# Kernel tuning notes

Measured on AMD Instinct MI355X. Metric: run time of the kernel, lower is better.

## Reference

```python
import jax, jax.numpy as jnp
import numpy as np

H = 64          # HIDDEN_DIM
V = 64          # VOCAB_SIZE
SLOTS = 8       # MEMORY_SLOTS
B, L = 256, 2048
LN_EPS = 1e-5
THRESH = 1.5    # entropy_threshold


def setup_inputs() -> dict:
    key = jax.random.key(0)
    ks = jax.random.split(key, 14)
    s = 0.05
    return {
        "seq": jax.random.randint(ks[0], (B, L), 0, V),
        "embed": jax.random.normal(ks[1], (V, H), jnp.float32) * s,
        "w1": jax.random.normal(ks[2], (H, 2 * H), jnp.float32) * s,
        "b1": jax.random.normal(ks[3], (2 * H,), jnp.float32) * s,
        "w2": jax.random.normal(ks[4], (2 * H, H), jnp.float32) * s,
        "b2": jax.random.normal(ks[5], (H,), jnp.float32) * s,
        "ln_g": jnp.ones((H,), jnp.float32),
        "ln_b": jnp.zeros((H,), jnp.float32),
        "gate_w": jax.random.normal(ks[6], (H, 1), jnp.float32) * s,
        "gate_b": jax.random.normal(ks[7], (1,), jnp.float32) * s,
        "q_w": jax.random.normal(ks[8], (H, H), jnp.float32) * s,
        "q_b": jax.random.normal(ks[9], (H,), jnp.float32) * s,
        "out_w": jax.random.normal(ks[10], (H, V), jnp.float32) * s,
        "out_b": jax.random.normal(ks[11], (V,), jnp.float32) * s,
    }


def reference(seq, embed, w1, b1, w2, b2, ln_g, ln_b,
              gate_w, gate_b, q_w, q_b, out_w, out_b):
    # Encoder: embed + FFN residual + LayerNorm
    h0 = embed[seq]                                      # [B, L, H]
    ff = jnp.maximum(h0 @ w1 + b1, 0.0) @ w2 + b2        # [B, L, H]
    z = h0 + ff
    mu = z.mean(-1, keepdims=True)
    var = z.var(-1, keepdims=True)
    h = (z - mu) / jnp.sqrt(var + LN_EPS) * ln_g + ln_b  # [B, L, H]

    # Top-k gate scores -> gather memory slots
    scores = (h @ gate_w)[..., 0] + gate_b[0]            # [B, L]
    _, idx = jax.lax.top_k(scores, SLOTS)                # [B, SLOTS]
    memory = jnp.take_along_axis(h, idx[:, :, None], axis=1)  # [B, SLOTS, H]

    # Tiny attention from last-token query over memory slots
    q = h[:, -1, :] @ q_w + q_b                          # [B, H]
    logits_attn = jnp.einsum('bkh,bh->bk', memory, q) / (H ** 0.5)
    attn = jax.nn.softmax(logits_attn, axis=-1)          # [B, SLOTS]

    # Entropy gate: fall back to uniform attention when entropy is high
    entropy = -(attn * jnp.log(attn + 1e-9)).sum(-1)     # [B]
    high = (entropy > THRESH).astype(attn.dtype)[:, None]
    eff_attn = (1.0 - high) * attn + high * (1.0 / SLOTS)

    ctx = jnp.einsum('bk,bkh->bh', eff_attn, memory)     # [B, H]
    logits = ctx @ out_w + out_b                         # [B, V]
    return logits, entropy.mean()
```

## Files before the change

### kernel.cpp

```cpp
#include <hip/hip_runtime.h>

#define HID 64
#define VOC 64
#define NSLOT 8
#define NB 256
#define SEQL 2048

__global__ __launch_bounds__(64) void vocab_kernel(
    const float* __restrict__ embed, const float* __restrict__ w1, const float* __restrict__ b1,
    const float* __restrict__ w2, const float* __restrict__ b2,
    const float* __restrict__ ln_g, const float* __restrict__ ln_b,
    const float* __restrict__ gate_w, const float* __restrict__ gate_b,
    const float* __restrict__ q_w, const float* __restrict__ q_b,
    float* __restrict__ wsH, float* __restrict__ wsQ, float* __restrict__ wsScore,
    float* __restrict__ ent_out)
{
    const int lane = threadIdx.x;
    const int v = blockIdx.x;

    if (v == 0 && lane == 0) ent_out[0] = 0.0f;

    const float e = embed[v * HID + lane];

    float fa = b1[lane], fb = b1[HID + lane];
#pragma unroll
    for (int i = 0; i < HID; ++i) {
        const float ei = __shfl(e, i);
        fa = fmaf(ei, w1[i * 2 * HID + lane], fa);
        fb = fmaf(ei, w1[i * 2 * HID + HID + lane], fb);
    }
    fa = fmaxf(fa, 0.0f);
    fb = fmaxf(fb, 0.0f);

    float za = e + b2[lane], zb = 0.0f;
#pragma unroll
    for (int j = 0; j < HID; ++j) {
        za = fmaf(__shfl(fa, j), w2[j * HID + lane], za);
        zb = fmaf(__shfl(fb, j), w2[(HID + j) * HID + lane], zb);
    }
    const float z = za + zb;

    float s = z;
#pragma unroll
    for (int m = 32; m; m >>= 1) s += __shfl_xor(s, m);
    const float mu = s * (1.0f / HID);
    const float d = z - mu;
    float vs = d * d;
#pragma unroll
    for (int m = 32; m; m >>= 1) vs += __shfl_xor(vs, m);
    const float inv = 1.0f / sqrtf(vs * (1.0f / HID) + 1e-5f);
    const float h = d * inv * ln_g[lane] + ln_b[lane];
    wsH[v * HID + lane] = h;

    float sc = h * gate_w[lane];
#pragma unroll
    for (int m = 32; m; m >>= 1) sc += __shfl_xor(sc, m);
    if (lane == 0) wsScore[v] = sc + gate_b[0];

    float q = q_b[lane];
#pragma unroll
    for (int k = 0; k < HID; ++k)
        q = fmaf(__shfl(h, k), q_w[k * HID + lane], q);
    wsQ[v * HID + lane] = q;
}

__global__ __launch_bounds__(256) void batch_kernel(
    const int* __restrict__ seq,
    const float* __restrict__ out_w, const float* __restrict__ out_b,
    const float* __restrict__ wsH, const float* __restrict__ wsQ,
    const float* __restrict__ wsScore,
    float* __restrict__ out, float* __restrict__ ent_out)
{
    __shared__ int hist[VOC];
    __shared__ float sscore[VOC];
    __shared__ float hlds[VOC * (HID + 1)];
    __shared__ float sqv[HID];
    __shared__ int sorder[VOC];
    __shared__ int svids[NSLOT];
    __shared__ float sla[NSLOT];
    __shared__ float seff[NSLOT];
    __shared__ int shvlast;

    const int t = threadIdx.x;
    const int b = blockIdx.x;

    if (t < VOC) { hist[t] = 0; sscore[t] = wsScore[t]; }
    if (t == 0) shvlast = seq[(size_t)b * SEQL + SEQL - 1];
    __syncthreads();

    const int4* row4 = (const int4*)(seq + (size_t)b * SEQL);
    for (int p = t; p < SEQL / 4; p += 256) {
        const int4 vv = row4[p];
        atomicAdd(&hist[vv.x], 1);
        atomicAdd(&hist[vv.y], 1);
        atomicAdd(&hist[vv.z], 1);
        atomicAdd(&hist[vv.w], 1);
    }
    for (int p = t; p < VOC * HID; p += 256)
        hlds[(p >> 6) * (HID + 1) + (p & 63)] = wsH[p];
    __syncthreads();

    if (t < VOC) {
        const float sv = sscore[t];
        int r = 0;
        for (int u = 0; u < VOC; ++u) {
            const float su = sscore[u];
            if (su > sv || (su == sv && u < t)) ++r;
        }
        sorder[r] = t;
        sqv[t] = wsQ[shvlast * HID + t];
    }
    __syncthreads();

    if (t == 0) {
        int r = NSLOT, n = 0, pos = 0;
        while (r > 0) {
            const int v = sorder[pos++];
            int c = hist[v];
            if (c > r) c = r;
            for (int k = 0; k < c; ++k) svids[n++] = v;
            r -= c;
        }
    }
    __syncthreads();

    if (t < NSLOT) {
        const float* hr = &hlds[svids[t] * (HID + 1)];
        float acc = 0.0f;
#pragma unroll
        for (int i = 0; i < HID; ++i) acc = fmaf(hr[i], sqv[i], acc);
        sla[t] = acc * 0.125f;
    }
    __syncthreads();

    if (t == 0) {
        float m = -1e30f;
        for (int k = 0; k < NSLOT; ++k) m = fmaxf(m, sla[k]);
        float e[NSLOT], s = 0.0f;
        for (int k = 0; k < NSLOT; ++k) { e[k] = expf(sla[k] - m); s += e[k]; }
        const float invs = 1.0f / s;
        float ent = 0.0f;
        for (int k = 0; k < NSLOT; ++k) {
            const float a = e[k] * invs;
            ent -= a * logf(a + 1e-9f);
        }
        const float high = (ent > 1.5f) ? 1.0f : 0.0f;
        for (int k = 0; k < NSLOT; ++k)
            seff[k] = (1.0f - high) * (e[k] * invs) + high * (1.0f / NSLOT);
        atomicAdd(ent_out, ent * (1.0f / NB));
    }
    __syncthreads();

    if (t < VOC) {
        float ctx = 0.0f;
#pragma unroll
        for (int k = 0; k < NSLOT; ++k)
            ctx = fmaf(seff[k], hlds[svids[k] * (HID + 1) + t], ctx);
        float acc = out_b[t];
#pragma unroll
        for (int i = 0; i < HID; ++i)
            acc = fmaf(__shfl(ctx, i), out_w[i * VOC + t], acc);
        out[(size_t)b * VOC + t] = acc;
    }
}

extern "C" void kernel_launch(void* const* d_in, const int* in_sizes, int n_in,
                              void* d_out, int out_size, void* d_ws, size_t ws_size,
                              hipStream_t stream) {
    const int*   seq    = (const int*)  d_in[0];
    const float* embed  = (const float*)d_in[1];
    const float* w1     = (const float*)d_in[2];
    const float* b1     = (const float*)d_in[3];
    const float* w2     = (const float*)d_in[4];
    const float* b2     = (const float*)d_in[5];
    const float* ln_g   = (const float*)d_in[6];
    const float* ln_b   = (const float*)d_in[7];
    const float* gate_w = (const float*)d_in[8];
    const float* gate_b = (const float*)d_in[9];
    const float* q_w    = (const float*)d_in[10];
    const float* q_b    = (const float*)d_in[11];
    const float* out_w  = (const float*)d_in[12];
    const float* out_b  = (const float*)d_in[13];
    float* out = (float*)d_out;
    float* ent_out = out + (size_t)NB * VOC;

    float* ws      = (float*)d_ws;
    float* wsH     = ws;
    float* wsQ     = ws + 4096;
    float* wsScore = ws + 8192;

    vocab_kernel<<<VOC, 64, 0, stream>>>(embed, w1, b1, w2, b2, ln_g, ln_b,
                                         gate_w, gate_b, q_w, q_b,
                                         wsH, wsQ, wsScore, ent_out);
    batch_kernel<<<NB, 256, 0, stream>>>(seq, out_w, out_b, wsH, wsQ, wsScore,
                                         out, ent_out);
}
```

Baseline: 23.95 us.

## Fuse vocab precompute into per-batch kernel and replace histogram with ranked counting

Merges the two kernels into one: each of the 256 blocks recomputes the 64-entry vocab encoder (FFN, LayerNorm, gate scores) in shared memory instead of reading precomputed workspace. The per-block histogram atomics are replaced by iterating vocab entries in score order and counting matches with wave reductions until 8 slots are filled. A memset now zeroes the entropy accumulator. This removes the inter-kernel dependency and one launch, at the cost of redundant encoder work in every block and a serial loop with several barriers per vocab entry.

```diff
diff --git a/kernel.cpp b/kernel.cpp
--- a/kernel.cpp
+++ b/kernel.cpp
@@ -5,99 +5,108 @@
 #define NSLOT 8
 #define NB 256
 #define SEQL 2048
-
-__global__ __launch_bounds__(64) void vocab_kernel(
+#define NT 512
+#define NW (NT / 64)
+#define EPAD 65
+#define FPAD 129
+
+__global__ __launch_bounds__(NT) void fused_kernel(
+    const int* __restrict__ seq,
     const float* __restrict__ embed, const float* __restrict__ w1, const float* __restrict__ b1,
     const float* __restrict__ w2, const float* __restrict__ b2,
     const float* __restrict__ ln_g, const float* __restrict__ ln_b,
     const float* __restrict__ gate_w, const float* __restrict__ gate_b,
     const float* __restrict__ q_w, const float* __restrict__ q_b,
-    float* __restrict__ wsH, float* __restrict__ wsQ, float* __restrict__ wsScore,
-    float* __restrict__ ent_out)
-{
-    const int lane = threadIdx.x;
-    const int v = blockIdx.x;
-
-    if (v == 0 && lane == 0) ent_out[0] = 0.0f;
-
-    const float e = embed[v * HID + lane];
-
-    float fa = b1[lane], fb = b1[HID + lane];
-#pragma unroll
-    for (int i = 0; i < HID; ++i) {
-        const float ei = __shfl(e, i);
-        fa = fmaf(ei, w1[i * 2 * HID + lane], fa);
-        fb = fmaf(ei, w1[i * 2 * HID + HID + lane], fb);
-    }
-    fa = fmaxf(fa, 0.0f);
-    fb = fmaxf(fb, 0.0f);
-
-    float za = e + b2[lane], zb = 0.0f;
-#pragma unroll
-    for (int j = 0; j < HID; ++j) {
-        za = fmaf(__shfl(fa, j), w2[j * HID + lane], za);
-        zb = fmaf(__shfl(fb, j), w2[(HID + j) * HID + lane], zb);
-    }
-    const float z = za + zb;
-
-    float s = z;
-#pragma unroll
-    for (int m = 32; m; m >>= 1) s += __shfl_xor(s, m);
-    const float mu = s * (1.0f / HID);
-    const float d = z - mu;
-    float vs = d * d;
-#pragma unroll
-    for (int m = 32; m; m >>= 1) vs += __shfl_xor(vs, m);
-    const float inv = 1.0f / sqrtf(vs * (1.0f / HID) + 1e-5f);
-    const float h = d * inv * ln_g[lane] + ln_b[lane];
-    wsH[v * HID + lane] = h;
-
-    float sc = h * gate_w[lane];
-#pragma unroll
-    for (int m = 32; m; m >>= 1) sc += __shfl_xor(sc, m);
-    if (lane == 0) wsScore[v] = sc + gate_b[0];
-
-    float q = q_b[lane];
-#pragma unroll
-    for (int k = 0; k < HID; ++k)
-        q = fmaf(__shfl(h, k), q_w[k * HID + lane], q);
-    wsQ[v * HID + lane] = q;
-}
-
-__global__ __launch_bounds__(256) void batch_kernel(
-    const int* __restrict__ seq,
     const float* __restrict__ out_w, const float* __restrict__ out_b,
-    const float* __restrict__ wsH, const float* __restrict__ wsQ,
-    const float* __restrict__ wsScore,
     float* __restrict__ out, float* __restrict__ ent_out)
 {
-    __shared__ int hist[VOC];
+    __shared__ float semb[VOC * EPAD];
+    __shared__ float sff[VOC * FPAD];
     __shared__ float sscore[VOC];
-    __shared__ float hlds[VOC * (HID + 1)];
+    __shared__ int   sorder[VOC];
     __shared__ float sqv[HID];
-    __shared__ int sorder[VOC];
-    __shared__ int svids[NSLOT];
+    __shared__ float sctx[HID];
+    __shared__ int   svids[NSLOT];
     __shared__ float sla[NSLOT];
     __shared__ float seff[NSLOT];
-    __shared__ int shvlast;
+    __shared__ int   scw[NW];
+    __shared__ int   s_u, s_rem, s_nv;
+    __shared__ int   shvlast;
 
     const int t = threadIdx.x;
     const int b = blockIdx.x;
-
-    if (t < VOC) { hist[t] = 0; sscore[t] = wsScore[t]; }
-    if (t == 0) shvlast = seq[(size_t)b * SEQL + SEQL - 1];
-    __syncthreads();
-
-    const int4* row4 = (const int4*)(seq + (size_t)b * SEQL);
-    for (int p = t; p < SEQL / 4; p += 256) {
-        const int4 vv = row4[p];
-        atomicAdd(&hist[vv.x], 1);
-        atomicAdd(&hist[vv.y], 1);
-        atomicAdd(&hist[vv.z], 1);
-        atomicAdd(&hist[vv.w], 1);
-    }
-    for (int p = t; p < VOC * HID; p += 256)
-        hlds[(p >> 6) * (HID + 1) + (p & 63)] = wsH[p];
+    const int lane = t & 63;
+    const int wave = t >> 6;
+
+    const int4 a = ((const int4*)(seq + (size_t)b * SEQL))[t];
+
+    for (int p = t; p < VOC * HID; p += NT)
+        semb[(p >> 6) * EPAD + (p & 63)] = embed[p];
+    if (t == 0) { s_rem = NSLOT; s_nv = 0; }
+    if (t == NT - 1) shvlast = a.w;
+    __syncthreads();
+
+    {
+        const int jb = __builtin_amdgcn_readfirstlane(wave * 16);
+        float acc[16];
+#pragma unroll
+        for (int jj = 0; jj < 16; ++jj) acc[jj] = b1[jb + jj];
+#pragma unroll 4
+        for (int i = 0; i < HID; ++i) {
+            const float ev = semb[lane * EPAD + i];
+            const float* wr = w1 + i * 2 * HID + jb;
+#pragma unroll
+            for (int jj = 0; jj < 16; ++jj)
+                acc[jj] = fmaf(ev, wr[jj], acc[jj]);
+        }
+#pragma unroll
+        for (int jj = 0; jj < 16; ++jj)
+            sff[lane * FPAD + jb + jj] = fmaxf(acc[jj], 0.0f);
+    }
+    __syncthreads();
+
+    {
+        const int ib = __builtin_amdgcn_readfirstlane(wave * 8);
+        float zacc[8];
+#pragma unroll
+        for (int ii = 0; ii < 8; ++ii) zacc[ii] = b2[ib + ii];
+#pragma unroll 4
+        for (int j = 0; j < 2 * HID; ++j) {
+            const float fv = sff[lane * FPAD + j];
+            const float* wr = w2 + j * HID + ib;
+#pragma unroll
+            for (int ii = 0; ii < 8; ++ii)
+                zacc[ii] = fmaf(fv, wr[ii], zacc[ii]);
+        }
+#pragma unroll
+        for (int ii = 0; ii < 8; ++ii)
+            semb[lane * EPAD + ib + ii] += zacc[ii];
+    }
+    __syncthreads();
+
+    {
+        const float lng = ln_g[lane], lnb = ln_b[lane], gw = gate_w[lane];
+        const int rbase = wave * 8;
+        for (int rr = 0; rr < 8; ++rr) {
+            const int r = rbase + rr;
+            const float z = semb[r * EPAD + lane];
+            float s = z;
+#pragma unroll
+            for (int m = 32; m; m >>= 1) s += __shfl_xor(s, m);
+            const float mu = s * (1.0f / HID);
+            const float d = z - mu;
+            float vs = d * d;
+#pragma unroll
+            for (int m = 32; m; m >>= 1) vs += __shfl_xor(vs, m);
+            const float inv = 1.0f / sqrtf(vs * (1.0f / HID) + 1e-5f);
+            const float h = d * inv * lng + lnb;
+            sff[r * FPAD + lane] = h;
+            float sc = h * gw;
+#pragma unroll
+            for (int m = 32; m; m >>= 1) sc += __shfl_xor(sc, m);
+            if (lane == 0) sscore[r] = sc + gate_b[0];
+        }
+    }
     __syncthreads();
 
     if (t < VOC) {
@@ -108,28 +117,49 @@
             if (su > sv || (su == sv && u < t)) ++r;
         }
         sorder[r] = t;
-        sqv[t] = wsQ[shvlast * HID + t];
-    }
-    __syncthreads();
-
-    if (t == 0) {
-        int r = NSLOT, n = 0, pos = 0;
-        while (r > 0) {
-            const int v = sorder[pos++];
-            int c = hist[v];
-            if (c > r) c = r;
-            for (int k = 0; k < c; ++k) svids[n++] = v;
-            r -= c;
-        }
-    }
-    __syncthreads();
-
-    if (t < NSLOT) {
-        const float* hr = &hlds[svids[t] * (HID + 1)];
-        float acc = 0.0f;
-#pragma unroll
-        for (int i = 0; i < HID; ++i) acc = fmaf(hr[i], sqv[i], acc);
-        sla[t] = acc * 0.125f;
+    }
+    __syncthreads();
+
+    for (int pos = 0; pos < VOC; ++pos) {
+        if (t == 0) s_u = sorder[pos];
+        __syncthreads();
+        const int u = s_u;
+        int c = (a.x == u) + (a.y == u) + (a.z == u) + (a.w == u);
+#pragma unroll
+        for (int m = 32; m; m >>= 1) c += __shfl_xor(c, m);
+        if (lane == 0) scw[wave] = c;
+        __syncthreads();
+        if (t == 0) {
+            int tot = 0;
+            for (int w = 0; w < NW; ++w) tot += scw[w];
+            int take = tot < s_rem ? tot : s_rem;
+            for (int k = 0; k < take; ++k) svids[s_nv++] = u;
+            s_rem -= take;
+        }
+        __syncthreads();
+        if (s_rem == 0) break;
+    }
+
+    const int vlast = shvlast;
+    if (t < HID) {
+        float qa = q_b[t];
+        for (int k = 0; k < HID; ++k)
+            qa = fmaf(sff[vlast * FPAD + k], q_w[k * HID + t], qa);
+        sqv[t] = qa;
+    }
+    __syncthreads();
+
+    if (t < VOC) {
+        const int k = t >> 3, e = t & 7;
+        const float* hr = &sff[svids[k] * FPAD];
+        float p = 0.0f;
+#pragma unroll
+        for (int m = 0; m < 8; ++m)
+            p = fmaf(hr[e + 8 * m], sqv[e + 8 * m], p);
+        p += __shfl_xor(p, 1);
+        p += __shfl_xor(p, 2);
+        p += __shfl_xor(p, 4);
+        if (e == 0) sla[k] = p * 0.125f;
     }
     __syncthreads();
 
@@ -141,8 +171,8 @@
         const float invs = 1.0f / s;
         float ent = 0.0f;
         for (int k = 0; k < NSLOT; ++k) {
-            const float a = e[k] * invs;
-            ent -= a * logf(a + 1e-9f);
+            const float av = e[k] * invs;
+            ent -= av * logf(av + 1e-9f);
         }
         const float high = (ent > 1.5f) ? 1.0f : 0.0f;
         for (int k = 0; k < NSLOT; ++k)
@@ -151,16 +181,19 @@
     }
     __syncthreads();
 
+    if (t < HID) {
+        float cx = 0.0f;
+#pragma unroll
+        for (int k = 0; k < NSLOT; ++k)
+            cx = fmaf(seff[k], sff[svids[k] * FPAD + t], cx);
+        sctx[t] = cx;
+    }
+    __syncthreads();
     if (t < VOC) {
-        float ctx = 0.0f;
-#pragma unroll
-        for (int k = 0; k < NSLOT; ++k)
-            ctx = fmaf(seff[k], hlds[svids[k] * (HID + 1) + t], ctx);
-        float acc = out_b[t];
-#pragma unroll
+        float o = out_b[t];
         for (int i = 0; i < HID; ++i)
-            acc = fmaf(__shfl(ctx, i), out_w[i * VOC + t], acc);
-        out[(size_t)b * VOC + t] = acc;
+            o = fmaf(sctx[i], out_w[i * VOC + t], o);
+        out[(size_t)b * VOC + t] = o;
     }
 }
 
@@ -184,14 +217,8 @@
     float* out = (float*)d_out;
     float* ent_out = out + (size_t)NB * VOC;
 
-    float* ws      = (float*)d_ws;
-    float* wsH     = ws;
-    float* wsQ     = ws + 4096;
-    float* wsScore = ws + 8192;
-
-    vocab_kernel<<<VOC, 64, 0, stream>>>(embed, w1, b1, w2, b2, ln_g, ln_b,
-                                         gate_w, gate_b, q_w, q_b,
-                                         wsH, wsQ, wsScore, ent_out);
-    batch_kernel<<<NB, 256, 0, stream>>>(seq, out_w, out_b, wsH, wsQ, wsScore,
-                                         out, ent_out);
+    hipMemsetAsync(ent_out, 0, sizeof(float), stream);
+    fused_kernel<<<NB, NT, 0, stream>>>(seq, embed, w1, b1, w2, b2, ln_g, ln_b,
+                                        gate_w, gate_b, q_w, q_b, out_w, out_b,
+                                        out, ent_out);
 }
```

Result: slower. 34.90 us (+45.7%).
